# Kernel tuning notes

Measured on AMD Instinct MI355X. Metric: run time of the kernel, lower is better.

Reference implementation:

```python
import jax, jax.numpy as jnp
import numpy as np
import math

F, M, C, OUT = 60, 600, 8, 18  # feature_size, max_samples, cluster_size, output_dim
B = 2048


def l2_normalize(x, axis):
    # matches tf.nn.l2_normalize (epsilon=1e-12)
    sq = jnp.sum(jnp.square(x), axis=axis, keepdims=True)
    return x * jax.lax.rsqrt(jnp.maximum(sq, 1e-12))


def setup_inputs() -> dict:
    key = jax.random.key(0)
    k = jax.random.split(key, 6)
    s1 = 1.0 / math.sqrt(F)
    s2 = 1.0 / math.sqrt(C)
    return {
        "reshaped_input": jax.random.normal(k[0], (B * M, F), dtype=jnp.float32),
        "cluster_weights": jax.random.normal(k[1], (F, C), dtype=jnp.float32) * s1,
        "covar_weights": jax.random.normal(k[2], (F, C), dtype=jnp.float32) * s1,
        "cluster_biases": jax.random.normal(k[3], (C,), dtype=jnp.float32) * s1,
        "cluster_weights2": jax.random.normal(k[4], (1, F, C), dtype=jnp.float32) * s1,
        "hidden1_weights": jax.random.normal(k[5], (2 * C * F, OUT), dtype=jnp.float32) * s2,
    }


def reference(reshaped_input, cluster_weights, covar_weights, cluster_biases,
              cluster_weights2, hidden1_weights):
    cw = jnp.square(covar_weights) + 1e-6                      # [F, C]

    act = reshaped_input @ cluster_weights + cluster_biases    # [B*M, C]
    act = jax.nn.softmax(act, axis=-1)
    act = act.reshape(-1, M, C)                                # [B, M, C]

    a_sum = jnp.sum(act, axis=-2, keepdims=True)               # [B, 1, C]
    a = a_sum * cluster_weights2                               # [B, F, C]

    x = reshaped_input.reshape(-1, M, F)                       # [B, M, F]

    fv1 = jnp.einsum('bmc,bmf->bfc', act, x)                   # [B, F, C]
    fv2 = jnp.einsum('bmc,bmf->bfc', act, jnp.square(x))       # [B, F, C]

    a2 = a_sum * jnp.square(cluster_weights2)                  # [B, F, C]
    b2 = fv1 * cluster_weights2                                # [B, F, C]

    fv2 = a2 + fv2 - 2.0 * b2
    fv2 = fv2 / jnp.square(cw)
    fv2 = fv2 - a_sum                                          # broadcast [B,1,C]
    fv2 = fv2.reshape(-1, C * F)
    fv2 = l2_normalize(fv2, axis=1)
    fv2 = l2_normalize(fv2, axis=1)  # second normalize as in original (idempotent)

    fv1 = (fv1 - a) / cw                                       # [B, F, C]
    fv1 = l2_normalize(fv1, axis=1)                            # per-cluster, along F
    fv1 = fv1.reshape(-1, C * F)
    fv1 = l2_normalize(fv1, axis=1)

    fv = jnp.concatenate([fv1, fv2], axis=1)                   # [B, 2*C*F]
    return fv @ hidden1_weights                                # [B, OUT]
```

## Files before the change

### kernel.cpp

```cpp
#include <hip/hip_runtime.h>

#define FDIM 60
#define MROW 600
#define CDIM 8
#define ODIM 18
#define CH   120
#define NCHUNK 5
#define BLK  512

__global__ void __launch_bounds__(BLK) netfv_kernel(
    const float* __restrict__ x,
    const float* __restrict__ W,
    const float* __restrict__ covar,
    const float* __restrict__ bias,
    const float* __restrict__ cw2,
    const float* __restrict__ H,
    float* __restrict__ out)
{
    __shared__ __align__(16) float xs[CH * 68];
    __shared__ __align__(16) float actl[CH * CDIM];
    __shared__ __align__(16) float Wt[CDIM * 64];
    __shared__ float biasl[CDIM];
    __shared__ float redA[64];
    __shared__ float redB[64];
    __shared__ float asuml[CDIM];
    __shared__ float n1rs[CDIM];
    __shared__ float n1c_s[CDIM], n2c_s[CDIM];
    __shared__ float scal[2];
    __shared__ __align__(16) float fvl[2 * FDIM * CDIM];

    const int tid  = threadIdx.x;
    const int b    = blockIdx.x;
    const int lane = tid & 63;
    const int wv   = tid >> 6;

    if (tid < FDIM * CDIM) {
        int f = tid >> 3, c = tid & 7;
        Wt[c * 64 + f] = W[tid];
    }
    if (tid < CDIM) biasl[tid] = bias[tid];

    const int r_ab  = tid >> 2;
    const int q_ab  = tid & 3;
    const int f0_ab = q_ab * 16;
    const int nv_ab = (q_ab == 3) ? 3 : 4;

    const int sss  = tid >> 7;
    const int tt   = tid & 127;
    const int c_c  = tt >> 4;
    const int fq_c = tt & 15;
    const bool actC = (fq_c < 15);
    const int f0_c = fq_c * 4;
    const int r0_c = sss * 30;

    float4 a1 = {0.f, 0.f, 0.f, 0.f}, a2 = {0.f, 0.f, 0.f, 0.f};
    float asum0 = 0.f, asum1 = 0.f;

    __syncthreads();

    float bl[8];
    #pragma unroll
    for (int c = 0; c < 8; ++c) bl[c] = biasl[c];

    const size_t rowbase = (size_t)b * (MROW * FDIM);

    for (int ck = 0; ck < NCHUNK; ++ck) {
        if (tid < 480) {
            const float* rp = x + rowbase + (size_t)(ck * CH + r_ab) * FDIM + f0_ab;
            float xv[16];
            #pragma unroll
            for (int v = 0; v < 4; ++v) {
                if (v < nv_ab) {
                    float4 u = ((const float4*)rp)[v];
                    xv[4*v+0] = u.x; xv[4*v+1] = u.y;
                    xv[4*v+2] = u.z; xv[4*v+3] = u.w;
                } else {
                    xv[4*v+0] = xv[4*v+1] = xv[4*v+2] = xv[4*v+3] = 0.f;
                }
            }
            #pragma unroll
            for (int v = 0; v < 4; ++v) {
                if (v < nv_ab)
                    *(float4*)&xs[r_ab * 68 + f0_ab + 4*v] =
                        make_float4(xv[4*v], xv[4*v+1], xv[4*v+2], xv[4*v+3]);
            }
            float lg[8];
            #pragma unroll
            for (int c = 0; c < 8; ++c) lg[c] = 0.f;
            #pragma unroll
            for (int c = 0; c < 8; ++c) {
                #pragma unroll
                for (int v = 0; v < 4; ++v) {
                    if (v < nv_ab) {
                        float4 w4 = *(const float4*)&Wt[c * 64 + f0_ab + 4*v];
                        lg[c] = fmaf(xv[4*v+0], w4.x, lg[c]);
                        lg[c] = fmaf(xv[4*v+1], w4.y, lg[c]);
                        lg[c] = fmaf(xv[4*v+2], w4.z, lg[c]);
                        lg[c] = fmaf(xv[4*v+3], w4.w, lg[c]);
                    }
                }
            }
            #pragma unroll
            for (int c = 0; c < 8; ++c) {
                lg[c] += __shfl_xor(lg[c], 1);
                lg[c] += __shfl_xor(lg[c], 2);
                lg[c] += bl[c];
            }
            float mx = lg[0];
            #pragma unroll
            for (int c = 1; c < 8; ++c) mx = fmaxf(mx, lg[c]);
            float s = 0.f;
            #pragma unroll
            for (int c = 0; c < 8; ++c) { lg[c] = __expf(lg[c] - mx); s += lg[c]; }
            float inv = 1.0f / s;
            float av0 = lg[2*q_ab] * inv, av1 = lg[2*q_ab+1] * inv;
            *(float2*)&actl[r_ab * 8 + 2*q_ab] = make_float2(av0, av1);
            asum0 += av0; asum1 += av1;
        }
        __syncthreads();
        if (actC) {
            #pragma unroll 5
            for (int rr = 0; rr < 30; ++rr) {
                int r = r0_c + rr;
                float av = actl[r * 8 + c_c];
                float4 xv4 = *(const float4*)&xs[r * 68 + f0_c];
                float t0 = av * xv4.x, t1 = av * xv4.y, t2 = av * xv4.z, t3 = av * xv4.w;
                a1.x += t0; a1.y += t1; a1.z += t2; a1.w += t3;
                a2.x = fmaf(t0, xv4.x, a2.x); a2.y = fmaf(t1, xv4.y, a2.y);
                a2.z = fmaf(t2, xv4.z, a2.z); a2.w = fmaf(t3, xv4.w, a2.w);
            }
        }
        __syncthreads();
    }

    {
        float v0 = asum0, v1 = asum1;
        v0 += __shfl_down(v0, 4);  v1 += __shfl_down(v1, 4);
        v0 += __shfl_down(v0, 8);  v1 += __shfl_down(v1, 8);
        v0 += __shfl_down(v0, 16); v1 += __shfl_down(v1, 16);
        v0 += __shfl_down(v0, 32); v1 += __shfl_down(v1, 32);
        if (lane < 4) { redA[wv * 8 + 2*lane] = v0; redA[wv * 8 + 2*lane + 1] = v1; }
    }
    __syncthreads();
    if (tid < 64) {
        float v = redA[tid];
        v += __shfl_down(v, 8); v += __shfl_down(v, 16); v += __shfl_down(v, 32);
        if (tid < 8) asuml[tid] = v;
    }
    __syncthreads();

    float* red8 = xs;
    *(float4*)&red8[tid * 8 + 0] = a1;
    *(float4*)&red8[tid * 8 + 4] = a2;
    __syncthreads();

    float fv1v = 0.f, fv2v = 0.f;
    const int f_e = tid >> 3, c_e = tid & 7;
    if (tid < 480) {
        int fq = f_e >> 2, j = f_e & 3;
        float fv1r = 0.f, fv2r = 0.f;
        #pragma unroll
        for (int s = 0; s < 4; ++s) {
            int bsx = (s * 128 + c_e * 16 + fq) * 8;
            fv1r += red8[bsx + j];
            fv2r += red8[bsx + 4 + j];
        }
        float asv  = asuml[c_e];
        float cw2v = cw2[f_e * 8 + c_e];
        float cv   = covar[f_e * 8 + c_e];
        float cwv  = cv * cv + 1e-6f;
        float rcw  = 1.0f / cwv;
        fv1v = (fv1r - asv * cw2v) * rcw;
        fv2v = (fmaf(asv * cw2v, cw2v, fv2r) - 2.0f * fv1r * cw2v) * rcw * rcw - asv;
    }

    {
        float p1 = fv1v * fv1v, p2 = fv2v * fv2v;
        p1 += __shfl_down(p1, 8);  p2 += __shfl_down(p2, 8);
        p1 += __shfl_down(p1, 16); p2 += __shfl_down(p2, 16);
        p1 += __shfl_down(p1, 32); p2 += __shfl_down(p2, 32);
        if (lane < 8) { redA[wv * 8 + lane] = p1; redB[wv * 8 + lane] = p2; }
    }
    __syncthreads();
    if (tid < 64) {
        float q1 = redA[tid], q2 = redB[tid];
        q1 += __shfl_down(q1, 8);  q2 += __shfl_down(q2, 8);
        q1 += __shfl_down(q1, 16); q2 += __shfl_down(q2, 16);
        q1 += __shfl_down(q1, 32); q2 += __shfl_down(q2, 32);
        if (tid < 8) { n1c_s[tid] = q1; n2c_s[tid] = q2; }
    }
    __syncthreads();
    if (tid == 0) {
        float S1 = 0.f, S2 = 0.f;
        #pragma unroll
        for (int c = 0; c < 8; ++c) {
            float rs = rsqrtf(fmaxf(n1c_s[c], 1e-12f));
            n1rs[c] = rs;
            S1 += n1c_s[c] * rs * rs;
            S2 += n2c_s[c];
        }
        scal[0] = rsqrtf(fmaxf(S1, 1e-12f));
        scal[1] = rsqrtf(fmaxf(S2, 1e-12f));
    }
    __syncthreads();
    if (tid < 480) {
        float fv1f = fv1v * n1rs[c_e] * scal[0];
        float fv2f = fv2v * scal[1];
        fvl[f_e * 8 + c_e]       = fv1f;
        fvl[480 + f_e * 8 + c_e] = fv2f;
    }
    __syncthreads();

    for (int o = wv; o < ODIM; o += 8) {
        float sacc = 0.f;
        #pragma unroll 5
        for (int i = lane; i < 960; i += 64)
            sacc = fmaf(fvl[i], H[i * ODIM + o], sacc);
        sacc += __shfl_down(sacc, 32);
        sacc += __shfl_down(sacc, 16);
        sacc += __shfl_down(sacc, 8);
        sacc += __shfl_down(sacc, 4);
        sacc += __shfl_down(sacc, 2);
        sacc += __shfl_down(sacc, 1);
        if (lane == 0) out[(size_t)b * ODIM + o] = sacc;
    }
}

extern "C" void kernel_launch(void* const* d_in, const int* in_sizes, int n_in,
                              void* d_out, int out_size, void* d_ws, size_t ws_size,
                              hipStream_t stream) {
    const float* x     = (const float*)d_in[0];
    const float* W     = (const float*)d_in[1];
    const float* covar = (const float*)d_in[2];
    const float* bias  = (const float*)d_in[3];
    const float* cw2   = (const float*)d_in[4];
    const float* H     = (const float*)d_in[5];
    float* outp = (float*)d_out;

    const int Bn = in_sizes[0] / (MROW * FDIM);
    hipLaunchKernelGGL(netfv_kernel, dim3(Bn), dim3(BLK), 0, stream,
                       x, W, covar, bias, cw2, H, outp);
}
```

Measured before the change: 449.5 us.

## Compute fv1/fv2 weighted sums with bf16 MFMA over transposed swizzled LDS tiles

Replaces the scalar FMA accumulation of act-weighted x and x^2 sums with bf16 MFMA 16x16x32 instructions. x and x^2 are packed to bf16 into transposed, XOR-swizzled LDS tiles, and activations go into a padded transposed buffer. The logits/softmax mapping changes to two rows per thread with an 8-lane reduction, and the chunk size moves to 128 rows, with the tail rows masked. Rounding x, x^2 and the activations to bf16 lowers the precision of the Fisher-vector sums. The loop was likely bound by global loads, so the compute savings may matter less.

```diff
diff --git a/kernel.cpp b/kernel.cpp
--- a/kernel.cpp
+++ b/kernel.cpp
@@ -4,11 +4,21 @@
 #define MROW 600
 #define CDIM 8
 #define ODIM 18
-#define CH   120
+#define CH   128
 #define NCHUNK 5
 #define BLK  512
 
-__global__ void __launch_bounds__(BLK) netfv_kernel(
+typedef short bf16x8 __attribute__((ext_vector_type(8)));
+typedef float f32x4  __attribute__((ext_vector_type(4)));
+
+__device__ __forceinline__ unsigned int packrne2(float lo, float hi) {
+    unsigned int ul = __float_as_uint(lo), uh = __float_as_uint(hi);
+    ul = (ul + 0x7fffu + ((ul >> 16) & 1u)) >> 16;
+    uh = (uh + 0x7fffu + ((uh >> 16) & 1u)) & 0xffff0000u;
+    return (ul & 0xffffu) | uh;
+}
+
+__global__ void __launch_bounds__(BLK, 4) netfv_kernel(
     const float* __restrict__ x,
     const float* __restrict__ W,
     const float* __restrict__ covar,
@@ -17,129 +27,134 @@
     const float* __restrict__ H,
     float* __restrict__ out)
 {
-    __shared__ __align__(16) float xs[CH * 68];
-    __shared__ __align__(16) float actl[CH * CDIM];
-    __shared__ __align__(16) float Wt[CDIM * 64];
-    __shared__ float biasl[CDIM];
-    __shared__ float redA[64];
-    __shared__ float redB[64];
-    __shared__ float asuml[CDIM];
-    __shared__ float n1rs[CDIM];
-    __shared__ float n1c_s[CDIM], n2c_s[CDIM];
-    __shared__ float scal[2];
-    __shared__ __align__(16) float fvl[2 * FDIM * CDIM];
+    __shared__ __align__(16) short xsT1[64 * 136];
+    __shared__ __align__(16) short xsT2[64 * 136];
+    __shared__ __align__(16) short actT[16 * 136];
+    __shared__ __align__(16) float Wt[8 * 64];
+    __shared__ __align__(16) float fvbuf[1024];
+    __shared__ __align__(16) float fvl[960];
+    __shared__ float redA[64], redB[64];
+    __shared__ float asuml[8], n1rs[8], n1c_s[8], n2c_s[8], scal[2];
 
     const int tid  = threadIdx.x;
     const int b    = blockIdx.x;
     const int lane = tid & 63;
     const int wv   = tid >> 6;
-
-    if (tid < FDIM * CDIM) {
-        int f = tid >> 3, c = tid & 7;
-        Wt[c * 64 + f] = W[tid];
-    }
-    if (tid < CDIM) biasl[tid] = bias[tid];
-
-    const int r_ab  = tid >> 2;
-    const int q_ab  = tid & 3;
-    const int f0_ab = q_ab * 16;
-    const int nv_ab = (q_ab == 3) ? 3 : 4;
-
-    const int sss  = tid >> 7;
-    const int tt   = tid & 127;
-    const int c_c  = tt >> 4;
-    const int fq_c = tt & 15;
-    const bool actC = (fq_c < 15);
-    const int f0_c = fq_c * 4;
-    const int r0_c = sss * 30;
-
-    float4 a1 = {0.f, 0.f, 0.f, 0.f}, a2 = {0.f, 0.f, 0.f, 0.f};
-    float asum0 = 0.f, asum1 = 0.f;
-
-    __syncthreads();
-
+    const int mg   = tid >> 3;
+    const int fs   = tid & 7;
+
+    { int c = tid >> 6, f = tid & 63; Wt[c * 64 + f] = (f < FDIM) ? W[f * 8 + c] : 0.f; }
+    {
+        unsigned int* az = (unsigned int*)(actT + 8 * 136);
+        for (int i = tid; i < 544; i += BLK) az[i] = 0u;
+    }
     float bl[8];
     #pragma unroll
-    for (int c = 0; c < 8; ++c) bl[c] = biasl[c];
+    for (int c = 0; c < 8; ++c) bl[c] = bias[c];
+
+    const int fvsel = wv & 1;
+    const int tile  = wv >> 1;
+    const int ln15  = lane & 15;
+    const int quad  = lane >> 4;
+    f32x4 acc = {0.f, 0.f, 0.f, 0.f};
+    float asum_l = 0.f;
+
+    __syncthreads();
 
     const size_t rowbase = (size_t)b * (MROW * FDIM);
 
     for (int ck = 0; ck < NCHUNK; ++ck) {
-        if (tid < 480) {
-            const float* rp = x + rowbase + (size_t)(ck * CH + r_ab) * FDIM + f0_ab;
-            float xv[16];
-            #pragma unroll
-            for (int v = 0; v < 4; ++v) {
-                if (v < nv_ab) {
-                    float4 u = ((const float4*)rp)[v];
-                    xv[4*v+0] = u.x; xv[4*v+1] = u.y;
-                    xv[4*v+2] = u.z; xv[4*v+3] = u.w;
-                } else {
-                    xv[4*v+0] = xv[4*v+1] = xv[4*v+2] = xv[4*v+3] = 0.f;
-                }
-            }
-            #pragma unroll
-            for (int v = 0; v < 4; ++v) {
-                if (v < nv_ab)
-                    *(float4*)&xs[r_ab * 68 + f0_ab + 4*v] =
-                        make_float4(xv[4*v], xv[4*v+1], xv[4*v+2], xv[4*v+3]);
-            }
-            float lg[8];
-            #pragma unroll
-            for (int c = 0; c < 8; ++c) lg[c] = 0.f;
+        const int r0  = 2 * mg;
+        const int r0g = ck * CH + r0;
+        const bool valid = (r0g < MROW);
+
+        float xv0[8], xv1[8];
+        float act0 = 0.f, act1 = 0.f;
+        if (valid) {
+            const float* p0 = x + rowbase + (size_t)r0g * FDIM + 8 * fs;
+            const float* p1 = p0 + FDIM;
+            float4 A0 = *(const float4*)p0;
+            float4 A1 = *(const float4*)p1;
+            float4 B0 = {0.f,0.f,0.f,0.f}, B1 = {0.f,0.f,0.f,0.f};
+            if (fs < 7) { B0 = *(const float4*)(p0 + 4); B1 = *(const float4*)(p1 + 4); }
+            xv0[0]=A0.x; xv0[1]=A0.y; xv0[2]=A0.z; xv0[3]=A0.w;
+            xv0[4]=B0.x; xv0[5]=B0.y; xv0[6]=B0.z; xv0[7]=B0.w;
+            xv1[0]=A1.x; xv1[1]=A1.y; xv1[2]=A1.z; xv1[3]=A1.w;
+            xv1[4]=B1.x; xv1[5]=B1.y; xv1[6]=B1.z; xv1[7]=B1.w;
+
+            float lg0[8], lg1[8];
             #pragma unroll
             for (int c = 0; c < 8; ++c) {
-                #pragma unroll
-                for (int v = 0; v < 4; ++v) {
-                    if (v < nv_ab) {
-                        float4 w4 = *(const float4*)&Wt[c * 64 + f0_ab + 4*v];
-                        lg[c] = fmaf(xv[4*v+0], w4.x, lg[c]);
-                        lg[c] = fmaf(xv[4*v+1], w4.y, lg[c]);
-                        lg[c] = fmaf(xv[4*v+2], w4.z, lg[c]);
-                        lg[c] = fmaf(xv[4*v+3], w4.w, lg[c]);
-                    }
-                }
+                float4 w0 = *(const float4*)&Wt[c * 64 + 8 * fs];
+                float4 w1 = *(const float4*)&Wt[c * 64 + 8 * fs + 4];
+                float s0 = 0.f, s1 = 0.f;
+                s0 = fmaf(xv0[0], w0.x, s0); s0 = fmaf(xv0[1], w0.y, s0);
+                s0 = fmaf(xv0[2], w0.z, s0); s0 = fmaf(xv0[3], w0.w, s0);
+                s0 = fmaf(xv0[4], w1.x, s0); s0 = fmaf(xv0[5], w1.y, s0);
+                s0 = fmaf(xv0[6], w1.z, s0); s0 = fmaf(xv0[7], w1.w, s0);
+                s1 = fmaf(xv1[0], w0.x, s1); s1 = fmaf(xv1[1], w0.y, s1);
+                s1 = fmaf(xv1[2], w0.z, s1); s1 = fmaf(xv1[3], w0.w, s1);
+                s1 = fmaf(xv1[4], w1.x, s1); s1 = fmaf(xv1[5], w1.y, s1);
+                s1 = fmaf(xv1[6], w1.z, s1); s1 = fmaf(xv1[7], w1.w, s1);
+                lg0[c] = s0; lg1[c] = s1;
             }
             #pragma unroll
             for (int c = 0; c < 8; ++c) {
-                lg[c] += __shfl_xor(lg[c], 1);
-                lg[c] += __shfl_xor(lg[c], 2);
-                lg[c] += bl[c];
-            }
-            float mx = lg[0];
-            #pragma unroll
-            for (int c = 1; c < 8; ++c) mx = fmaxf(mx, lg[c]);
-            float s = 0.f;
-            #pragma unroll
-            for (int c = 0; c < 8; ++c) { lg[c] = __expf(lg[c] - mx); s += lg[c]; }
-            float inv = 1.0f / s;
-            float av0 = lg[2*q_ab] * inv, av1 = lg[2*q_ab+1] * inv;
-            *(float2*)&actl[r_ab * 8 + 2*q_ab] = make_float2(av0, av1);
-            asum0 += av0; asum1 += av1;
+                lg0[c] += __shfl_xor(lg0[c], 1);
+                lg0[c] += __shfl_xor(lg0[c], 2);
+                lg0[c] += __shfl_xor(lg0[c], 4);
+                lg1[c] += __shfl_xor(lg1[c], 1);
+                lg1[c] += __shfl_xor(lg1[c], 2);
+                lg1[c] += __shfl_xor(lg1[c], 4);
+                lg0[c] += bl[c]; lg1[c] += bl[c];
+            }
+            float mx0 = lg0[0], mx1 = lg1[0];
+            #pragma unroll
+            for (int c = 1; c < 8; ++c) { mx0 = fmaxf(mx0, lg0[c]); mx1 = fmaxf(mx1, lg1[c]); }
+            float s0 = 0.f, s1 = 0.f;
+            #pragma unroll
+            for (int c = 0; c < 8; ++c) {
+                lg0[c] = __expf(lg0[c] - mx0); s0 += lg0[c];
+                lg1[c] = __expf(lg1[c] - mx1); s1 += lg1[c];
+            }
+            float i0 = 1.f / s0, i1 = 1.f / s1;
+            #pragma unroll
+            for (int c = 0; c < 8; ++c)
+                if (c == fs) { act0 = lg0[c] * i0; act1 = lg1[c] * i1; }
+            asum_l += act0 + act1;
+        }
+        ((unsigned int*)actT)[fs * 68 + mg] = valid ? packrne2(act0, act1) : 0u;
+        if (valid) {
+            const int wbase = (((mg >> 2) ^ fs) << 2) + (mg & 3);
+            #pragma unroll
+            for (int i = 0; i < 8; ++i) {
+                int f = 8 * fs + i;
+                int woff = f * 68 + wbase;
+                ((unsigned int*)xsT1)[woff] = packrne2(xv0[i], xv1[i]);
+                ((unsigned int*)xsT2)[woff] = packrne2(xv0[i] * xv0[i], xv1[i] * xv1[i]);
+            }
         }
         __syncthreads();
-        if (actC) {
-            #pragma unroll 5
-            for (int rr = 0; rr < 30; ++rr) {
-                int r = r0_c + rr;
-                float av = actl[r * 8 + c_c];
-                float4 xv4 = *(const float4*)&xs[r * 68 + f0_c];
-                float t0 = av * xv4.x, t1 = av * xv4.y, t2 = av * xv4.z, t3 = av * xv4.w;
-                a1.x += t0; a1.y += t1; a1.z += t2; a1.w += t3;
-                a2.x = fmaf(t0, xv4.x, a2.x); a2.y = fmaf(t1, xv4.y, a2.y);
-                a2.z = fmaf(t2, xv4.z, a2.z); a2.w = fmaf(t3, xv4.w, a2.w);
+
+        {
+            const short* xsel = fvsel ? xsT2 : xsT1;
+            const int f   = tile * 16 + ln15;
+            const int fsw = f >> 3;
+            #pragma unroll
+            for (int ks = 0; ks < 4; ++ks) {
+                bf16x8 av = *(const bf16x8*)(actT + ln15 * 136 + ks * 32 + quad * 8);
+                int kblk = ks * 4 + quad;
+                bf16x8 bv = *(const bf16x8*)(xsel + f * 136 + ((kblk ^ fsw) << 3));
+                acc = __builtin_amdgcn_mfma_f32_16x16x32_bf16(av, bv, acc, 0, 0, 0);
             }
         }
         __syncthreads();
     }
 
     {
-        float v0 = asum0, v1 = asum1;
-        v0 += __shfl_down(v0, 4);  v1 += __shfl_down(v1, 4);
-        v0 += __shfl_down(v0, 8);  v1 += __shfl_down(v1, 8);
-        v0 += __shfl_down(v0, 16); v1 += __shfl_down(v1, 16);
-        v0 += __shfl_down(v0, 32); v1 += __shfl_down(v1, 32);
-        if (lane < 4) { redA[wv * 8 + 2*lane] = v0; redA[wv * 8 + 2*lane + 1] = v1; }
+        float v = asum_l;
+        v += __shfl_down(v, 8); v += __shfl_down(v, 16); v += __shfl_down(v, 32);
+        if (lane < 8) redA[wv * 8 + lane] = v;
     }
     __syncthreads();
     if (tid < 64) {
@@ -147,24 +162,21 @@
         v += __shfl_down(v, 8); v += __shfl_down(v, 16); v += __shfl_down(v, 32);
         if (tid < 8) asuml[tid] = v;
     }
-    __syncthreads();
-
-    float* red8 = xs;
-    *(float4*)&red8[tid * 8 + 0] = a1;
-    *(float4*)&red8[tid * 8 + 4] = a2;
+    if (quad < 2) {
+        #pragma unroll
+        for (int r = 0; r < 4; ++r) {
+            int c = quad * 4 + r;
+            int f = tile * 16 + ln15;
+            fvbuf[fvsel * 512 + f * 8 + c] = acc[r];
+        }
+    }
     __syncthreads();
 
     float fv1v = 0.f, fv2v = 0.f;
     const int f_e = tid >> 3, c_e = tid & 7;
     if (tid < 480) {
-        int fq = f_e >> 2, j = f_e & 3;
-        float fv1r = 0.f, fv2r = 0.f;
-        #pragma unroll
-        for (int s = 0; s < 4; ++s) {
-            int bsx = (s * 128 + c_e * 16 + fq) * 8;
-            fv1r += red8[bsx + j];
-            fv2r += red8[bsx + 4 + j];
-        }
+        float fv1r = fvbuf[f_e * 8 + c_e];
+        float fv2r = fvbuf[512 + f_e * 8 + c_e];
         float asv  = asuml[c_e];
         float cw2v = cw2[f_e * 8 + c_e];
         float cv   = covar[f_e * 8 + c_e];
@@ -204,10 +216,8 @@
     }
     __syncthreads();
     if (tid < 480) {
-        float fv1f = fv1v * n1rs[c_e] * scal[0];
-        float fv2f = fv2v * scal[1];
-        fvl[f_e * 8 + c_e]       = fv1f;
-        fvl[480 + f_e * 8 + c_e] = fv2f;
+        fvl[f_e * 8 + c_e]       = fv1v * n1rs[c_e] * scal[0];
+        fvl[480 + f_e * 8 + c_e] = fv2v * scal[1];
     }
     __syncthreads();
 
```

New measurement: 440.5 us. -2.0%, faster.
